# Optimization experiments

Hardware: AMD Instinct MI355X
Metric: run time of the kernel (lower is better)

## Reference

```python
import jax, jax.numpy as jnp
import numpy as np


def setup_inputs() -> dict:
    key = jax.random.key(0)
    k1, k2 = jax.random.split(key)
    B, C_in, H, Wd = 8, 64, 64, 64
    C_a = 32
    x = jax.random.normal(k1, (B, C_in, H, Wd), dtype=jnp.float32)
    # 1x1 conv == per-pixel linear map: weight [C_a, C_in], bias [C_a]
    W = jax.random.normal(k2, (C_a, C_in), dtype=jnp.float32) * (1.0 / np.sqrt(C_in))
    b = jnp.zeros((C_a,), dtype=jnp.float32)
    return {"x": x, "W": W, "b": b}


def reference(x, W, b):
    B, C, H, Wd = x.shape
    N = H * Wd
    # g = 1x1 conv: [B, C_a, H, W] -> flatten spatial -> [B, C_a, N]
    g = jnp.einsum('oc,bchw->bohw', W, x) + b[None, :, None, None]
    g = g.reshape(B, -1, N)
    # alpha[b, n, m] = softmax_m( sum_c g[b,c,n] * g[b,c,m] )  (unscaled)
    scores = jnp.einsum('bcn,bcm->bnm', g, g)
    alpha = jax.nn.softmax(scores, axis=2)
    # r[b, c, n] = sum_m alpha[b,n,m] * x[b,c,m]
    xf = x.reshape(B, C, N)
    r = jnp.einsum('bnm,bcm->bcn', alpha, xf)
    # residual (intended semantics of is_residual=True) + ReLU epilogue
    r = r + xf
    out = jax.nn.relu(r).reshape(B, C, H, Wd)
    return (out, alpha)
```

## Files before the change

### kernel.cpp

```cpp
#include <hip/hip_runtime.h>
#include <math.h>

#define BB 8
#define CC 64
#define NA 4096
#define KA 32
#define LOG2E 1.4426950408889634f

typedef short bfrag __attribute__((ext_vector_type(8)));
typedef int   i4    __attribute__((ext_vector_type(4)));
typedef float f4    __attribute__((ext_vector_type(4)));
typedef float f16v  __attribute__((ext_vector_type(16)));

__device__ __forceinline__ f16v mf(bfrag a, bfrag b, f16v c) {
    return __builtin_amdgcn_mfma_f32_32x32x16_bf16(a, b, c, 0, 0, 0);
}

__device__ __forceinline__ unsigned short bfrne(float f) {
    unsigned u = __builtin_bit_cast(unsigned, f);
    return (unsigned short)((u + 0x7FFFu + ((u >> 16) & 1u)) >> 16);
}
__device__ __forceinline__ unsigned pk2(float a, float b) {
    return (unsigned)bfrne(a) | ((unsigned)bfrne(b) << 16);
}
__device__ __forceinline__ float bf2f(unsigned short h) {
    unsigned u = ((unsigned)h) << 16;
    return __builtin_bit_cast(float, u);
}

__global__ __launch_bounds__(256) void k_g(const float* __restrict__ x,
                                           const float* __restrict__ W,
                                           const float* __restrict__ bias,
                                           short* __restrict__ ghi,
                                           short* __restrict__ glo,
                                           float* __restrict__ norms) {
    __shared__ float Wl[KA * CC];
    __shared__ float bl[KA];
    int tid = threadIdx.x;
    for (int i = tid; i < KA * CC; i += 256) Wl[i] = W[i];
    if (tid < KA) bl[tid] = bias[tid];
    __syncthreads();

    int b = blockIdx.y;
    int n = blockIdx.x * 256 + tid;

    float acc[KA];
#pragma unroll
    for (int k = 0; k < KA; k++) acc[k] = 0.f;

    const float* xp = x + (size_t)b * CC * NA + n;
#pragma unroll 4
    for (int c = 0; c < CC; c++) {
        float xv = xp[(size_t)c * NA];
#pragma unroll
        for (int k = 0; k < KA; k++) acc[k] = fmaf(Wl[k * CC + c], xv, acc[k]);
    }

    float ss = 0.f;
    unsigned ph[KA / 2], pl[KA / 2];
#pragma unroll
    for (int k = 0; k < KA; k += 2) {
        float v0 = acc[k] + bl[k];
        float v1 = acc[k + 1] + bl[k + 1];
        ss = fmaf(v0, v0, fmaf(v1, v1, ss));
        unsigned short h0 = bfrne(v0), h1 = bfrne(v1);
        float l0 = v0 - bf2f(h0), l1 = v1 - bf2f(h1);
        ph[k / 2] = (unsigned)h0 | ((unsigned)h1 << 16);
        pl[k / 2] = (unsigned)bfrne(l0) | ((unsigned)bfrne(l1) << 16);
    }
    norms[b * NA + n] = sqrtf(ss);

    size_t row = ((size_t)b * NA + n) * KA;
#pragma unroll
    for (int q = 0; q < 4; q++) {
        i4 vh = { (int)ph[4 * q], (int)ph[4 * q + 1], (int)ph[4 * q + 2], (int)ph[4 * q + 3] };
        i4 vl = { (int)pl[4 * q], (int)pl[4 * q + 1], (int)pl[4 * q + 2], (int)pl[4 * q + 3] };
        *(i4*)(ghi + row + q * 8) = vh;
        *(i4*)(glo + row + q * 8) = vl;
    }
}

__global__ __launch_bounds__(256) void k_gmax(const float* __restrict__ norms,
                                              float* __restrict__ gmaxp) {
    int b = blockIdx.x, tid = threadIdx.x;
    float m = 0.f;
    for (int i = tid; i < NA; i += 256) m = fmaxf(m, norms[b * NA + i]);
#pragma unroll
    for (int off = 1; off < 64; off <<= 1) m = fmaxf(m, __shfl_xor(m, off));
    __shared__ float red[4];
    if ((tid & 63) == 0) red[tid >> 6] = m;
    __syncthreads();
    if (tid == 0) gmaxp[b] = fmaxf(fmaxf(red[0], red[1]), fmaxf(red[2], red[3]));
}

__global__ __launch_bounds__(256) void k_xb(const float* __restrict__ x,
                                            short* __restrict__ xb) {
    size_t idx = ((size_t)blockIdx.x * 256 + threadIdx.x) * 4;
    f4 v = *(const f4*)(x + idx);
    int2 p;
    p.x = (int)pk2(v[0], v[1]);
    p.y = (int)pk2(v[2], v[3]);
    *(int2*)(xb + idx) = p;
}

__global__ __launch_bounds__(256, 4) void k_den(const short* __restrict__ ghi,
                                                const short* __restrict__ glo,
                                                const float* __restrict__ norms,
                                                const float* __restrict__ gmaxp,
                                                float* __restrict__ partial) {
    __shared__ float rowsum[4][32];
    const int tid = threadIdx.x;
    const int w = tid >> 6;
    const int l31 = tid & 31;
    const int hi = (tid >> 5) & 1;
    const int id = blockIdx.x;
    const int b = id & 7;
    const int rr = id >> 3;
    const int nb = rr & 127;
    const int mc = rr >> 7;
    const int n0 = nb * 32;

    const float C2 = -norms[b * NA + n0 + l31] * gmaxp[b] * LOG2E;
    const short* gh = ghi + (size_t)b * NA * KA;
    const short* gl = glo + (size_t)b * NA * KA;

    bfrag Bh[2], Bl[2];
#pragma unroll
    for (int kt = 0; kt < 2; kt++) {
        size_t o = (size_t)(n0 + l31) * KA + kt * 16 + hi * 8;
        Bh[kt] = *(const bfrag*)(gh + o);
        Bl[kt] = *(const bfrag*)(gl + o);
    }

    float ls = 0.f;
#pragma unroll 2
    for (int i = 0; i < 8; i++) {
        const int m0 = (mc * 8 + i) * 128 + w * 32;
        bfrag Ah[2], Al[2];
#pragma unroll
        for (int kt = 0; kt < 2; kt++) {
            size_t o = (size_t)(m0 + l31) * KA + kt * 16 + hi * 8;
            Ah[kt] = *(const bfrag*)(gh + o);
            Al[kt] = *(const bfrag*)(gl + o);
        }
        f16v sA = {}, sB = {};
        sA = mf(Ah[0], Bh[0], sA); sA = mf(Ah[1], Bh[1], sA);
        sB = mf(Ah[0], Bl[0], sB); sB = mf(Ah[1], Bl[1], sB);
        sB = mf(Al[0], Bh[0], sB); sB = mf(Al[1], Bh[1], sB);
#pragma unroll
        for (int r = 0; r < 16; r++) ls += exp2f(fmaf(sA[r] + sB[r], LOG2E, C2));
    }
    ls += __shfl_xor(ls, 32);
    if (hi == 0) rowsum[w][l31] = ls;
    __syncthreads();
    if (tid < 32)
        partial[((size_t)mc * BB + b) * NA + n0 + tid] =
            rowsum[0][tid] + rowsum[1][tid] + rowsum[2][tid] + rowsum[3][tid];
}

__global__ __launch_bounds__(256) void k_red(const float* __restrict__ partial,
                                             float* __restrict__ linv) {
    int i = blockIdx.x * 256 + threadIdx.x;
    const size_t S = (size_t)BB * NA;
    linv[i] = 1.f / (partial[i] + partial[S + i] + partial[2 * S + i] + partial[3 * S + i]);
}

__global__ __launch_bounds__(256, 3) void k_attn2(const float* __restrict__ x,
                                                  const short* __restrict__ ghi,
                                                  const short* __restrict__ glo,
                                                  const short* __restrict__ xb,
                                                  const float* __restrict__ norms,
                                                  const float* __restrict__ gmaxp,
                                                  const float* __restrict__ linv,
                                                  float* __restrict__ out,
                                                  float* __restrict__ alpha) {
    __shared__ __align__(16) char smem[34816 + 16384];
    short* xt = (short*)smem;
    float* ast = (float*)(smem + 34816);

    const int tid = threadIdx.x;
    const int w = tid >> 6;
    const int l31 = tid & 31;
    const int hi = (tid >> 5) & 1;
    const int id = blockIdx.x;
    const int b = id & 7;
    const int n0 = (id >> 3) * 32;

    const float M = norms[b * NA + n0 + l31] * gmaxp[b];
    const float C2 = -M * LOG2E;
    const float L = linv[b * NA + n0 + l31];

    const short* gh = ghi + (size_t)b * NA * KA;
    const short* gl = glo + (size_t)b * NA * KA;
    const short* xp = xb + (size_t)b * CC * NA;
    float* ap = alpha + (size_t)b * NA * NA;

    bfrag Bh[2], Bl[2];
#pragma unroll
    for (int kt = 0; kt < 2; kt++) {
        size_t o = (size_t)(n0 + l31) * KA + kt * 16 + hi * 8;
        Bh[kt] = *(const bfrag*)(gh + o);
        Bl[kt] = *(const bfrag*)(gl + o);
    }

    const int sc = tid >> 2, ss = tid & 3;

    i4 xs[4];
    {
        const short* src = xp + (size_t)sc * NA;
#pragma unroll
        for (int i = 0; i < 4; i++) xs[i] = *(const i4*)(src + ss * 32 + i * 8);
    }
    bfrag Ah[2], Al[2];
#pragma unroll
    for (int kt = 0; kt < 2; kt++) {
        size_t o = (size_t)(w * 32 + l31) * KA + kt * 16 + hi * 8;
        Ah[kt] = *(const bfrag*)(gh + o);
        Al[kt] = *(const bfrag*)(gl + o);
    }
#pragma unroll
    for (int i = 0; i < 4; i++) *(i4*)(xt + sc * 136 + ss * 32 + i * 8) = xs[i];
    __syncthreads();

    f16v pv0 = {}, pv1 = {};
    int cur = 0;

    for (int it = 0; it < 32; ++it) {
        if (it < 31) {
            const short* src = xp + (size_t)sc * NA + (it + 1) * 128;
#pragma unroll
            for (int i = 0; i < 4; i++) xs[i] = *(const i4*)(src + ss * 32 + i * 8);
        }
        f16v sA = {}, sB = {};
        sA = mf(Ah[0], Bh[0], sA); sA = mf(Ah[1], Bh[1], sA);
        sB = mf(Ah[0], Bl[0], sB); sB = mf(Ah[1], Bl[1], sB);
        sB = mf(Al[0], Bh[0], sB); sB = mf(Al[1], Bh[1], sB);
        if (it < 31) {
            const int m0n = (it + 1) * 128 + w * 32;
#pragma unroll
            for (int kt = 0; kt < 2; kt++) {
                size_t o = (size_t)(m0n + l31) * KA + kt * 16 + hi * 8;
                Ah[kt] = *(const bfrag*)(gh + o);
                Al[kt] = *(const bfrag*)(gl + o);
            }
        }
        float a[16];
#pragma unroll
        for (int r = 0; r < 16; r++) a[r] = exp2f(fmaf(sA[r] + sB[r], LOG2E, C2)) * L;
#pragma unroll
        for (int q = 0; q < 4; q++) {
            f4 v = { a[4 * q], a[4 * q + 1], a[4 * q + 2], a[4 * q + 3] };
            int phys = (w * 8 + 2 * q + hi) ^ (l31 & 7);
            *(f4*)&ast[l31 * 128 + phys * 4] = v;
        }
        __syncthreads();

#pragma unroll
        for (int e = 0; e < 4; e++) {
            int row = e * 8 + (tid >> 5);
            int clog = tid & 31;
            int phys = clog ^ (row & 7);
            f4 v = *(const f4*)&ast[row * 128 + phys * 4];
            *(f4*)(ap + (size_t)(n0 + row) * NA + it * 128 + clog * 4) = v;
        }

        unsigned p0 = pk2(a[0], a[1]),   p1 = pk2(a[2], a[3]);
        unsigned p2 = pk2(a[4], a[5]),   p3 = pk2(a[6], a[7]);
        unsigned p4 = pk2(a[8], a[9]),   p5 = pk2(a[10], a[11]);
        unsigned p6 = pk2(a[12], a[13]), p7 = pk2(a[14], a[15]);
        asm("v_permlane32_swap_b32 %0, %1" : "+v"(p0), "+v"(p2));
        asm("v_permlane32_swap_b32 %0, %1" : "+v"(p1), "+v"(p3));
        asm("v_permlane32_swap_b32 %0, %1" : "+v"(p4), "+v"(p6));
        asm("v_permlane32_swap_b32 %0, %1" : "+v"(p5), "+v"(p7));
        i4 f0 = { (int)p0, (int)p1, (int)p2, (int)p3 };
        i4 f1 = { (int)p4, (int)p5, (int)p6, (int)p7 };
        bfrag pa0 = __builtin_bit_cast(bfrag, f0);
        bfrag pa1 = __builtin_bit_cast(bfrag, f1);

        const short* xc = xt + cur * 8704;
        bfrag X00 = *(const bfrag*)(xc + l31 * 136 + w * 32 + hi * 8);
        bfrag X01 = *(const bfrag*)(xc + l31 * 136 + w * 32 + hi * 8 + 16);
        pv0 = mf(pa0, X00, pv0); pv0 = mf(pa1, X01, pv0);
        bfrag X10 = *(const bfrag*)(xc + (32 + l31) * 136 + w * 32 + hi * 8);
        bfrag X11 = *(const bfrag*)(xc + (32 + l31) * 136 + w * 32 + hi * 8 + 16);
        pv1 = mf(pa0, X10, pv1); pv1 = mf(pa1, X11, pv1);

        if (it < 31) {
            short* xn = xt + (cur ^ 1) * 8704;
#pragma unroll
            for (int i = 0; i < 4; i++) *(i4*)(xn + sc * 136 + ss * 32 + i * 8) = xs[i];
        }
        __syncthreads();
        cur ^= 1;
    }

    float (*pvr0)[CC + 1] = (float(*)[CC + 1])smem;
    float (*pvr1)[CC + 1] = (float(*)[CC + 1])(smem + 32 * (CC + 1) * 4);
    if (w >= 2) {
        float (*buf)[CC + 1] = (w == 2) ? pvr0 : pvr1;
#pragma unroll
        for (int r = 0; r < 16; r++) {
            int nl = (r & 3) + 8 * (r >> 2) + 4 * hi;
            buf[nl][l31]      = pv0[r];
            buf[nl][32 + l31] = pv1[r];
        }
    }
    __syncthreads();
    if (w < 2) {
        float (*buf)[CC + 1] = (w == 0) ? pvr0 : pvr1;
#pragma unroll
        for (int r = 0; r < 16; r++) {
            int nl = (r & 3) + 8 * (r >> 2) + 4 * hi;
            buf[nl][l31]      += pv0[r];
            buf[nl][32 + l31] += pv1[r];
        }
    }
    __syncthreads();

    const float* xr = x + (size_t)b * CC * NA + n0;
    float* op = out + (size_t)b * CC * NA + n0;
#pragma unroll
    for (int e = 0; e < 8; e++) {
        int idx = e * 256 + tid;
        int c = idx >> 5, n = idx & 31;
        float v = pvr0[n][c] + pvr1[n][c] + xr[(size_t)c * NA + n];
        op[(size_t)c * NA + n] = fmaxf(v, 0.f);
    }
}

extern "C" void kernel_launch(void* const* d_in, const int* in_sizes, int n_in,
                              void* d_out, int out_size, void* d_ws, size_t ws_size,
                              hipStream_t stream) {
    const float* x = (const float*)d_in[0];
    const float* W = (const float*)d_in[1];
    const float* bias = (const float*)d_in[2];

    float* out = (float*)d_out;
    float* alpha = out + (size_t)BB * CC * NA;

    short* ghi = (short*)d_ws;
    short* glo = ghi + (size_t)BB * NA * KA;
    short* xb  = glo + (size_t)BB * NA * KA;
    float* norms = (float*)(xb + (size_t)BB * CC * NA);
    float* gmaxp = norms + (size_t)BB * NA;
    float* partial = gmaxp + BB;
    float* linv = partial + (size_t)4 * BB * NA;

    k_g<<<dim3(NA / 256, BB), 256, 0, stream>>>(x, W, bias, ghi, glo, norms);
    k_gmax<<<BB, 256, 0, stream>>>(norms, gmaxp);
    k_xb<<<(BB * CC * NA) / (256 * 4), 256, 0, stream>>>(x, xb);
    k_den<<<4096, 256, 0, stream>>>(ghi, glo, norms, gmaxp, partial);
    k_red<<<BB * NA / 256, 256, 0, stream>>>(partial, linv);
    k_attn2<<<1024, 256, 0, stream>>>(x, ghi, glo, xb, norms, gmaxp, linv, out, alpha);
}
```

Before: 222.0 us.

## Read x fragments directly from global and double-buffer wider alpha tiles

Removes the LDS staging of bf16 x tiles, so the PV MFMA B-operands are loaded straight from global memory. Each iteration now covers 256 columns in two sub-steps, and the alpha staging buffer is double-buffered so there is one barrier per iteration instead of two. Alpha rows are written with nontemporal stores, and the occupancy hint drops from 3 to 2 blocks. The aim is to cut barrier and LDS traffic on the store-bound alpha path. In exchange the global x loads are uncoalesced and latency-exposed, and occupancy is lower.

```diff
diff --git a/kernel.cpp b/kernel.cpp
--- a/kernel.cpp
+++ b/kernel.cpp
@@ -165,7 +165,7 @@
     linv[i] = 1.f / (partial[i] + partial[S + i] + partial[2 * S + i] + partial[3 * S + i]);
 }
 
-__global__ __launch_bounds__(256, 3) void k_attn2(const float* __restrict__ x,
+__global__ __launch_bounds__(256, 2) void k_attn2(const float* __restrict__ x,
                                                   const short* __restrict__ ghi,
                                                   const short* __restrict__ glo,
                                                   const short* __restrict__ xb,
@@ -174,9 +174,8 @@
                                                   const float* __restrict__ linv,
                                                   float* __restrict__ out,
                                                   float* __restrict__ alpha) {
-    __shared__ __align__(16) char smem[34816 + 16384];
-    short* xt = (short*)smem;
-    float* ast = (float*)(smem + 34816);
+    __shared__ __align__(16) char smem[2 * 32 * 256 * 4];
+    float* ast = (float*)smem;
 
     const int tid = threadIdx.x;
     const int w = tid >> 6;
@@ -203,96 +202,75 @@
         Bl[kt] = *(const bfrag*)(gl + o);
     }
 
-    const int sc = tid >> 2, ss = tid & 3;
-
-    i4 xs[4];
-    {
-        const short* src = xp + (size_t)sc * NA;
-#pragma unroll
-        for (int i = 0; i < 4; i++) xs[i] = *(const i4*)(src + ss * 32 + i * 8);
-    }
-    bfrag Ah[2], Al[2];
-#pragma unroll
-    for (int kt = 0; kt < 2; kt++) {
-        size_t o = (size_t)(w * 32 + l31) * KA + kt * 16 + hi * 8;
-        Ah[kt] = *(const bfrag*)(gh + o);
-        Al[kt] = *(const bfrag*)(gl + o);
-    }
-#pragma unroll
-    for (int i = 0; i < 4; i++) *(i4*)(xt + sc * 136 + ss * 32 + i * 8) = xs[i];
-    __syncthreads();
-
     f16v pv0 = {}, pv1 = {};
-    int cur = 0;
-
-    for (int it = 0; it < 32; ++it) {
-        if (it < 31) {
-            const short* src = xp + (size_t)sc * NA + (it + 1) * 128;
-#pragma unroll
-            for (int i = 0; i < 4; i++) xs[i] = *(const i4*)(src + ss * 32 + i * 8);
-        }
-        f16v sA = {}, sB = {};
-        sA = mf(Ah[0], Bh[0], sA); sA = mf(Ah[1], Bh[1], sA);
-        sB = mf(Ah[0], Bl[0], sB); sB = mf(Ah[1], Bl[1], sB);
-        sB = mf(Al[0], Bh[0], sB); sB = mf(Al[1], Bh[1], sB);
-        if (it < 31) {
-            const int m0n = (it + 1) * 128 + w * 32;
+
+    for (int it = 0; it < 16; ++it) {
+        float* astb = ast + (it & 1) * 8192;
+
+#pragma unroll
+        for (int sub = 0; sub < 2; ++sub) {
+            const int m0 = it * 256 + sub * 128 + w * 32;
+            bfrag Ah[2], Al[2];
 #pragma unroll
             for (int kt = 0; kt < 2; kt++) {
-                size_t o = (size_t)(m0n + l31) * KA + kt * 16 + hi * 8;
+                size_t o = (size_t)(m0 + l31) * KA + kt * 16 + hi * 8;
                 Ah[kt] = *(const bfrag*)(gh + o);
                 Al[kt] = *(const bfrag*)(gl + o);
             }
-        }
-        float a[16];
-#pragma unroll
-        for (int r = 0; r < 16; r++) a[r] = exp2f(fmaf(sA[r] + sB[r], LOG2E, C2)) * L;
-#pragma unroll
-        for (int q = 0; q < 4; q++) {
-            f4 v = { a[4 * q], a[4 * q + 1], a[4 * q + 2], a[4 * q + 3] };
-            int phys = (w * 8 + 2 * q + hi) ^ (l31 & 7);
-            *(f4*)&ast[l31 * 128 + phys * 4] = v;
-        }
+            f16v sA = {}, sB = {};
+            sA = mf(Ah[0], Bh[0], sA); sA = mf(Ah[1], Bh[1], sA);
+            sB = mf(Ah[0], Bl[0], sB); sB = mf(Ah[1], Bl[1], sB);
+            sB = mf(Al[0], Bh[0], sB); sB = mf(Al[1], Bh[1], sB);
+
+            float a[16];
+#pragma unroll
+            for (int r = 0; r < 16; r++) a[r] = exp2f(fmaf(sA[r] + sB[r], LOG2E, C2)) * L;
+
+#pragma unroll
+            for (int q = 0; q < 4; q++) {
+                f4 v = { a[4 * q], a[4 * q + 1], a[4 * q + 2], a[4 * q + 3] };
+                int phys = (w * 8 + 2 * q + hi) ^ (l31 & 7);
+                *(f4*)&astb[l31 * 256 + sub * 128 + phys * 4] = v;
+            }
+
+            unsigned p0 = pk2(a[0], a[1]),   p1 = pk2(a[2], a[3]);
+            unsigned p2 = pk2(a[4], a[5]),   p3 = pk2(a[6], a[7]);
+            unsigned p4 = pk2(a[8], a[9]),   p5 = pk2(a[10], a[11]);
+            unsigned p6 = pk2(a[12], a[13]), p7 = pk2(a[14], a[15]);
+            asm("v_permlane32_swap_b32 %0, %1" : "+v"(p0), "+v"(p2));
+            asm("v_permlane32_swap_b32 %0, %1" : "+v"(p1), "+v"(p3));
+            asm("v_permlane32_swap_b32 %0, %1" : "+v"(p4), "+v"(p6));
+            asm("v_permlane32_swap_b32 %0, %1" : "+v"(p5), "+v"(p7));
+            i4 f0 = { (int)p0, (int)p1, (int)p2, (int)p3 };
+            i4 f1 = { (int)p4, (int)p5, (int)p6, (int)p7 };
+            bfrag pa0 = __builtin_bit_cast(bfrag, f0);
+            bfrag pa1 = __builtin_bit_cast(bfrag, f1);
+
+            size_t ox0 = (size_t)l31 * NA + m0 + hi * 8;
+            size_t ox1 = (size_t)(32 + l31) * NA + m0 + hi * 8;
+            bfrag X00 = *(const bfrag*)(xp + ox0);
+            bfrag X01 = *(const bfrag*)(xp + ox0 + 16);
+            bfrag X10 = *(const bfrag*)(xp + ox1);
+            bfrag X11 = *(const bfrag*)(xp + ox1 + 16);
+
+            pv0 = mf(pa0, X00, pv0); pv0 = mf(pa1, X01, pv0);
+            pv1 = mf(pa0, X10, pv1); pv1 = mf(pa1, X11, pv1);
+        }
+
         __syncthreads();
 
 #pragma unroll
-        for (int e = 0; e < 4; e++) {
-            int row = e * 8 + (tid >> 5);
-            int clog = tid & 31;
-            int phys = clog ^ (row & 7);
-            f4 v = *(const f4*)&ast[row * 128 + phys * 4];
-            *(f4*)(ap + (size_t)(n0 + row) * NA + it * 128 + clog * 4) = v;
-        }
-
-        unsigned p0 = pk2(a[0], a[1]),   p1 = pk2(a[2], a[3]);
-        unsigned p2 = pk2(a[4], a[5]),   p3 = pk2(a[6], a[7]);
-        unsigned p4 = pk2(a[8], a[9]),   p5 = pk2(a[10], a[11]);
-        unsigned p6 = pk2(a[12], a[13]), p7 = pk2(a[14], a[15]);
-        asm("v_permlane32_swap_b32 %0, %1" : "+v"(p0), "+v"(p2));
-        asm("v_permlane32_swap_b32 %0, %1" : "+v"(p1), "+v"(p3));
-        asm("v_permlane32_swap_b32 %0, %1" : "+v"(p4), "+v"(p6));
-        asm("v_permlane32_swap_b32 %0, %1" : "+v"(p5), "+v"(p7));
-        i4 f0 = { (int)p0, (int)p1, (int)p2, (int)p3 };
-        i4 f1 = { (int)p4, (int)p5, (int)p6, (int)p7 };
-        bfrag pa0 = __builtin_bit_cast(bfrag, f0);
-        bfrag pa1 = __builtin_bit_cast(bfrag, f1);
-
-        const short* xc = xt + cur * 8704;
-        bfrag X00 = *(const bfrag*)(xc + l31 * 136 + w * 32 + hi * 8);
-        bfrag X01 = *(const bfrag*)(xc + l31 * 136 + w * 32 + hi * 8 + 16);
-        pv0 = mf(pa0, X00, pv0); pv0 = mf(pa1, X01, pv0);
-        bfrag X10 = *(const bfrag*)(xc + (32 + l31) * 136 + w * 32 + hi * 8);
-        bfrag X11 = *(const bfrag*)(xc + (32 + l31) * 136 + w * 32 + hi * 8 + 16);
-        pv1 = mf(pa0, X10, pv1); pv1 = mf(pa1, X11, pv1);
-
-        if (it < 31) {
-            short* xn = xt + (cur ^ 1) * 8704;
-#pragma unroll
-            for (int i = 0; i < 4; i++) *(i4*)(xn + sc * 136 + ss * 32 + i * 8) = xs[i];
-        }
-        __syncthreads();
-        cur ^= 1;
-    }
+        for (int e = 0; e < 8; e++) {
+            int flat = e * 256 + tid;
+            int row = flat >> 6;
+            int c4 = flat & 63;
+            int grp = c4 >> 5, c32 = c4 & 31;
+            int phys = c32 ^ (row & 7);
+            f4 v = *(const f4*)&astb[row * 256 + grp * 128 + phys * 4];
+            __builtin_nontemporal_store(v, (f4*)(ap + (size_t)(n0 + row) * NA + it * 256 + c4 * 4));
+        }
+    }
+    __syncthreads();
 
     float (*pvr0)[CC + 1] = (float(*)[CC + 1])smem;
     float (*pvr1)[CC + 1] = (float(*)[CC + 1])(smem + 32 * (CC + 1) * 4);
```

Measured after the change: 201.4 us. 1.1x faster.
